# Kernel optimization log

Measured on AMD Instinct MI355X. Metric: run time of the kernel, lower is better.

## Reference

```python
import jax, jax.numpy as jnp
import numpy as np

NEG_SLOPE = 0.2


def add_self_loops(edge_index, num_nodes):
    loop = jnp.arange(num_nodes, dtype=edge_index.dtype)
    src = jnp.concatenate([edge_index[0], loop])
    dst = jnp.concatenate([edge_index[1], loop])
    return src, dst


def gat_conv(x, src, dst, W, att_src, att_dst, bias, heads, out_ch, concat):
    N = x.shape[0]
    h = (x @ W).reshape(N, heads, out_ch)                      # [N,H,C]
    a_src = jnp.sum(h * att_src, axis=-1)                      # [N,H]
    a_dst = jnp.sum(h * att_dst, axis=-1)                      # [N,H]
    e = a_src[src] + a_dst[dst]                                # [E,H]
    e = jax.nn.leaky_relu(e, NEG_SLOPE)
    # segment softmax over incoming edges of each destination node
    m = jax.ops.segment_max(e, dst, num_segments=N)            # [N,H]
    m = jnp.where(jnp.isfinite(m), m, 0.0)
    ex = jnp.exp(e - m[dst])
    s = jax.ops.segment_sum(ex, dst, num_segments=N)           # [N,H]
    alpha = ex / jnp.where(s[dst] > 0, s[dst], 1.0)            # [E,H]
    msg = alpha[:, :, None] * h[src]                           # [E,H,C]
    out = jax.ops.segment_sum(msg, dst, num_segments=N)        # [N,H,C]
    if concat:
        out = out.reshape(N, heads * out_ch)
    else:
        out = out.mean(axis=1)
    return out + bias


def setup_inputs() -> dict:
    key = jax.random.key(0)
    ks = jax.random.split(key, 10)
    N, F, E, H, C1 = 50000, 128, 800000, 8, 8
    x = jax.random.normal(ks[0], (N, F), dtype=jnp.float32)
    edge_index = jax.random.randint(ks[1], (2, E), 0, N, dtype=jnp.int64)
    sc = 0.1
    W1 = jax.random.normal(ks[2], (F, H * C1), dtype=jnp.float32) * sc
    a_src1 = jax.random.normal(ks[3], (H, C1), dtype=jnp.float32) * sc
    a_dst1 = jax.random.normal(ks[4], (H, C1), dtype=jnp.float32) * sc
    b1 = jnp.zeros((H * C1,), dtype=jnp.float32)
    W2 = jax.random.normal(ks[5], (H * C1, F), dtype=jnp.float32) * sc
    a_src2 = jax.random.normal(ks[6], (1, F), dtype=jnp.float32) * sc
    a_dst2 = jax.random.normal(ks[7], (1, F), dtype=jnp.float32) * sc
    b2 = jnp.zeros((F,), dtype=jnp.float32)
    return {"x": x, "edge_index": edge_index, "W1": W1, "a_src1": a_src1,
            "a_dst1": a_dst1, "b1": b1, "W2": W2, "a_src2": a_src2,
            "a_dst2": a_dst2, "b2": b2}


def reference(x, edge_index, W1, a_src1, a_dst1, b1, W2, a_src2, a_dst2, b2):
    N = x.shape[0]
    src, dst = add_self_loops(edge_index, N)
    h = gat_conv(x, src, dst, W1, a_src1, a_dst1, b1, heads=8, out_ch=8, concat=True)
    h = jax.nn.elu(h)
    out = gat_conv(h, src, dst, W2, a_src2, a_dst2, b2, heads=1, out_ch=x.shape[1], concat=True)
    return out
```

## Files before the change

### kernel.cpp

```cpp
#include <hip/hip_runtime.h>
#include <hip/hip_fp16.h>
#include <math.h>

#define NEG_SLOPE 0.2f

typedef _Float16 f16x8 __attribute__((ext_vector_type(8)));
typedef float    f32x4 __attribute__((ext_vector_type(4)));

__device__ __forceinline__ void get_edge(const int* __restrict__ ei, int E, int e,
                                         int& s, int& d) {
    if (e < E) { s = ei[e]; d = ei[E + e]; }
    else       { s = e - E; d = e - E; }
}

union G1SMem {
    unsigned int sWu[4096];
    struct {
        int lhist[256], lbase[256], lrank[256];
        unsigned int sbuf[4096];
    } sc;
};

__global__ __launch_bounds__(256) void g1s_kernel(const float* __restrict__ x,
                                                  const float* __restrict__ W,
                                                  const float* __restrict__ asrc,
                                                  const float* __restrict__ adst,
                                                  _Float16* __restrict__ hout,
                                                  float* __restrict__ av,
                                                  float* __restrict__ bv, int N,
                                                  int gblocks,
                                                  const float* __restrict__ W2,
                                                  const float* __restrict__ as2,
                                                  const float* __restrict__ ad2,
                                                  float* __restrict__ wa,
                                                  float* __restrict__ wb,
                                                  const int* __restrict__ ei, int E, int ET,
                                                  unsigned int* __restrict__ bstore,
                                                  int* __restrict__ bofs) {
    __shared__ G1SMem sm;
    int t = threadIdx.x;

    if (blockIdx.x == (unsigned)gblocks) {
        if (t < 64) {
            const float* wr = W2 + t * 128;
            float sa = 0.f, sb = 0.f;
#pragma unroll 8
            for (int c = 0; c < 128; ++c) {
                float w = wr[c];
                sa = fmaf(w, as2[c], sa);
                sb = fmaf(w, ad2[c], sb);
            }
            wa[t] = sa; wb[t] = sb;
        }
        return;
    }

    if (blockIdx.x > (unsigned)gblocks) {
        int sblk = blockIdx.x - gblocks - 1;
        int start = sblk * 4096;
        int cnt = ET - start; if (cnt > 4096) cnt = 4096;
        sm.sc.lhist[t] = 0; sm.sc.lrank[t] = 0;
        __syncthreads();
        int mybuck[16]; unsigned int myval[16];
#pragma unroll
        for (int k = 0; k < 16; ++k) {
            int e = start + t + k * 256;
            mybuck[k] = -1;
            if (e < ET) {
                int s, d; get_edge(ei, E, e, s, d);
                mybuck[k] = d >> 8;
                myval[k] = ((unsigned int)(d & 255) << 16) | (unsigned int)s;
                atomicAdd(&sm.sc.lhist[mybuck[k]], 1);
            }
        }
        __syncthreads();
        int v = sm.sc.lhist[t];
        sm.sc.lbase[t] = v;
        __syncthreads();
        for (int off = 1; off < 256; off <<= 1) {
            int u = (t >= off) ? sm.sc.lbase[t - off] : 0;
            __syncthreads();
            sm.sc.lbase[t] += u;
            __syncthreads();
        }
        int excl = sm.sc.lbase[t] - v;
        bofs[(sblk << 8) + t] = excl;
        sm.sc.lbase[t] = excl;
        __syncthreads();
#pragma unroll
        for (int k = 0; k < 16; ++k) {
            int b = mybuck[k];
            if (b >= 0) {
                int r = atomicAdd(&sm.sc.lrank[b], 1);
                sm.sc.sbuf[sm.sc.lbase[b] + r] = myval[k];
            }
        }
        __syncthreads();
        for (int j = t; j < cnt; j += 256)
            bstore[start + j] = sm.sc.sbuf[j];
        return;
    }

    for (int p = t; p < 4096; p += 256) {
        int frag = p >> 8;
        int lane = (p >> 2) & 63;
        int j2   = p & 3;
        int chunk = frag >> 2, nt = frag & 3;
        int k = chunk * 32 + ((lane >> 4) << 3) + (j2 << 1);
        int n = nt * 16 + (lane & 15);
        union { _Float16 h[2]; unsigned int u; } pk;
        pk.h[0] = (_Float16)W[k * 64 + n];
        pk.h[1] = (_Float16)W[(k + 1) * 64 + n];
        sm.sWu[p] = pk.u;
    }
    __syncthreads();

    int lane = t & 63;
    int wid  = t >> 6;
    int rbase = blockIdx.x * 64 + wid * 16;
    int l15 = lane & 15, quad = lane >> 4;
    int rA = rbase + l15; if (rA >= N) rA = N - 1;

    const unsigned int* fragbase = &sm.sWu[lane * 4];
    f32x4 z = {0.f, 0.f, 0.f, 0.f};
    f32x4 acc[4] = {z, z, z, z};

#pragma unroll
    for (int chunk = 0; chunk < 4; ++chunk) {
        const float* xp = x + (size_t)rA * 128 + chunk * 32 + quad * 8;
        float4 f0 = *((const float4*)xp);
        float4 f1 = *((const float4*)(xp + 4));
        f16x8 af;
        af[0] = (_Float16)f0.x; af[1] = (_Float16)f0.y;
        af[2] = (_Float16)f0.z; af[3] = (_Float16)f0.w;
        af[4] = (_Float16)f1.x; af[5] = (_Float16)f1.y;
        af[6] = (_Float16)f1.z; af[7] = (_Float16)f1.w;
#pragma unroll
        for (int tt = 0; tt < 4; ++tt) {
            f16x8 bf = *((const f16x8*)(fragbase + (chunk * 4 + tt) * 256));
            acc[tt] = __builtin_amdgcn_mfma_f32_16x16x32_f16(af, bf, acc[tt], 0, 0, 0);
        }
    }

    float asc[4], adc[4];
#pragma unroll
    for (int tt = 0; tt < 4; ++tt) { asc[tt] = asrc[tt * 16 + l15]; adc[tt] = adst[tt * 16 + l15]; }
#pragma unroll
    for (int reg = 0; reg < 4; ++reg) {
        int r = rbase + quad * 4 + reg;
        bool ok = (r < N);
#pragma unroll
        for (int tt = 0; tt < 4; ++tt) {
            float v = acc[tt][reg];
            if (ok) hout[(size_t)r * 64 + tt * 16 + l15] = (_Float16)v;
            float pa = v * asc[tt], pb = v * adc[tt];
            pa += __shfl_xor(pa, 1); pb += __shfl_xor(pb, 1);
            pa += __shfl_xor(pa, 2); pb += __shfl_xor(pb, 2);
            pa += __shfl_xor(pa, 4); pb += __shfl_xor(pb, 4);
            if (ok && (lane & 7) == 0) {
                int head = tt * 2 + (l15 >> 3);
                av[r * 8 + head] = pa;
                bv[r * 8 + head] = pb;
            }
        }
    }
}

__device__ __forceinline__ void rank_quarter(const unsigned int* __restrict__ bstore,
                                             const int* __restrict__ bofs,
                                             int b, int q, int ET, int nblk,
                                             unsigned short (*colL)[64],
                                             int* lrank) {
    int t = threadIdx.x;
    if (t < 64) lrank[t] = 0;
    __syncthreads();
    int lane = t & 63, wid = t >> 6;
    for (int sblk = wid; sblk < nblk; sblk += 8) {
        int base = sblk << 12;
        int cnt = ET - base; if (cnt > 4096) cnt = 4096;
        int beg = bofs[(sblk << 8) + b];
        int end = (b < 255) ? bofs[(sblk << 8) + b + 1] : cnt;
        for (int i = beg + lane; i < end; i += 64) {
            unsigned int pk = bstore[base + i];
            int local = pk >> 16;
            if ((local >> 6) == q) {
                int r = atomicAdd(&lrank[local & 63], 1);
                if (r < 64) colL[local & 63][r] = (unsigned short)(pk & 0xFFFFu);
            }
        }
    }
    __syncthreads();
}

__global__ __launch_bounds__(512) void agg1_kernel(const unsigned int* __restrict__ bstore,
                                                   const int* __restrict__ bofs,
                                                   const float* __restrict__ av,
                                                   const float* __restrict__ bv,
                                                   const __half* __restrict__ h1,
                                                   const float* __restrict__ b1,
                                                   const float* __restrict__ wa,
                                                   const float* __restrict__ wb,
                                                   _Float16* __restrict__ out1,
                                                   float* __restrict__ av2,
                                                   float* __restrict__ bv2,
                                                   int N, int ET, int nblk) {
    __shared__ unsigned short colL[64][64];
    __shared__ int lrank[64];
    int blk = blockIdx.x;
    rank_quarter(bstore, bofs, blk >> 2, blk & 3, ET, nblk, colL, lrank);

    int lane = threadIdx.x & 63;
    int wid  = threadIdx.x >> 6;
    int g  = (lane >> 3) & 3;
    int gl = lane & 7;
    const uint4* hrow = (const uint4*)h1;
    uint4 z4 = {0u, 0u, 0u, 0u};

#pragma unroll 1
    for (int pass = 0; pass < 4; ++pass) {
        int nl = pass * 16 + wid * 2 + (lane >> 5);
        int node = blk * 64 + nl;
        bool valid = node < N;
        int nodeC = valid ? node : 0;
        int deg = lrank[nl]; if (deg > 64) deg = 64;
        int last = deg - 1; if (last < 0) last = 0;
        float bd = bv[nodeC * 8 + gl];

        int e = g;
        int c0 = colL[nl][e      <= last ? e      : last];
        int c1 = colL[nl][e + 4  <= last ? e + 4  : last];
        int c2 = colL[nl][e + 8  <= last ? e + 8  : last];
        float av0 = 0.f, av1v = 0.f; uint4 h0 = z4, h1v = z4;
        if (e < deg)     { av0  = av[c0 * 8 + gl]; h0  = hrow[(size_t)c0 * 8 + gl]; }
        if (e + 4 < deg) { av1v = av[c1 * 8 + gl]; h1v = hrow[(size_t)c1 * 8 + gl]; }

        float s = 0.f, a0 = 0.f, a1 = 0.f, a2 = 0.f, a3 = 0.f,
              a4 = 0.f, a5 = 0.f, a6 = 0.f, a7 = 0.f;
        for (; e < deg; e += 4) {
            float av2v = 0.f; uint4 h2 = z4;
            if (e + 8 < deg) { av2v = av[c2 * 8 + gl]; h2 = hrow[(size_t)c2 * 8 + gl]; }
            int c3 = colL[nl][e + 12 <= last ? e + 12 : last];
            float l = av0 + bd;
            l = l > 0.f ? l : NEG_SLOPE * l;
            float w = __expf(l);
            float2 f0 = __half22float2(*(const __half2*)&h0.x);
            float2 f1 = __half22float2(*(const __half2*)&h0.y);
            float2 f2 = __half22float2(*(const __half2*)&h0.z);
            float2 f3 = __half22float2(*(const __half2*)&h0.w);
            s += w;
            a0 = fmaf(w, f0.x, a0); a1 = fmaf(w, f0.y, a1);
            a2 = fmaf(w, f1.x, a2); a3 = fmaf(w, f1.y, a3);
            a4 = fmaf(w, f2.x, a4); a5 = fmaf(w, f2.y, a5);
            a6 = fmaf(w, f3.x, a6); a7 = fmaf(w, f3.y, a7);
            av0 = av1v; h0 = h1v; av1v = av2v; h1v = h2; c2 = c3;
        }
#pragma unroll
        for (int off = 8; off < 32; off <<= 1) {
            s  += __shfl_xor(s, off);
            a0 += __shfl_xor(a0, off); a1 += __shfl_xor(a1, off);
            a2 += __shfl_xor(a2, off); a3 += __shfl_xor(a3, off);
            a4 += __shfl_xor(a4, off); a5 += __shfl_xor(a5, off);
            a6 += __shfl_xor(a6, off); a7 += __shfl_xor(a7, off);
        }
        float inv = s > 0.f ? __builtin_amdgcn_rcpf(s) : 0.f;
        float4 bb0 = ((const float4*)b1)[gl * 2];
        float4 bb1 = ((const float4*)b1)[gl * 2 + 1];
        float v0 = a0 * inv + bb0.x, v1 = a1 * inv + bb0.y;
        float v2 = a2 * inv + bb0.z, v3 = a3 * inv + bb0.w;
        float v4 = a4 * inv + bb1.x, v5 = a5 * inv + bb1.y;
        float v6 = a6 * inv + bb1.z, v7 = a7 * inv + bb1.w;
        v0 = v0 > 0.f ? v0 : __expf(v0) - 1.f; v1 = v1 > 0.f ? v1 : __expf(v1) - 1.f;
        v2 = v2 > 0.f ? v2 : __expf(v2) - 1.f; v3 = v3 > 0.f ? v3 : __expf(v3) - 1.f;
        v4 = v4 > 0.f ? v4 : __expf(v4) - 1.f; v5 = v5 > 0.f ? v5 : __expf(v5) - 1.f;
        v6 = v6 > 0.f ? v6 : __expf(v6) - 1.f; v7 = v7 > 0.f ? v7 : __expf(v7) - 1.f;
        float4 wa0 = ((const float4*)wa)[gl * 2], wa1 = ((const float4*)wa)[gl * 2 + 1];
        float4 wb0 = ((const float4*)wb)[gl * 2], wb1 = ((const float4*)wb)[gl * 2 + 1];
        float pa = v0 * wa0.x + v1 * wa0.y + v2 * wa0.z + v3 * wa0.w
                 + v4 * wa1.x + v5 * wa1.y + v6 * wa1.z + v7 * wa1.w;
        float pb = v0 * wb0.x + v1 * wb0.y + v2 * wb0.z + v3 * wb0.w
                 + v4 * wb1.x + v5 * wb1.y + v6 * wb1.z + v7 * wb1.w;
        pa += __shfl_xor(pa, 1); pb += __shfl_xor(pb, 1);
        pa += __shfl_xor(pa, 2); pb += __shfl_xor(pb, 2);
        pa += __shfl_xor(pa, 4); pb += __shfl_xor(pb, 4);
        if (valid && (lane & 31) == 0) { av2[node] = pa; bv2[node] = pb; }
        if (valid && g == 0) {
            f16x8 o;
            o[0] = (_Float16)v0; o[1] = (_Float16)v1; o[2] = (_Float16)v2; o[3] = (_Float16)v3;
            o[4] = (_Float16)v4; o[5] = (_Float16)v5; o[6] = (_Float16)v6; o[7] = (_Float16)v7;
            ((f16x8*)out1)[(size_t)node * 8 + gl] = o;
        }
    }
}

union A2Mem {
    struct { unsigned short colL[64][64]; int lrank[64]; } rk;
    unsigned int sWu[4096];
};

__global__ __launch_bounds__(512) void agg2g2_kernel(const unsigned int* __restrict__ bstore,
                                                     const int* __restrict__ bofs,
                                                     const float* __restrict__ av,
                                                     const float* __restrict__ bv,
                                                     const __half* __restrict__ out1,
                                                     const float* __restrict__ W,
                                                     const float* __restrict__ b2,
                                                     float* __restrict__ dout,
                                                     int N, int ET, int nblk) {
    __shared__ A2Mem sm;
    __shared__ _Float16 sAgg[64][72];
    int blk = blockIdx.x;
    int t = threadIdx.x;
    int lane = t & 63;
    int wid  = t >> 6;
    int rbase = blk * 64;

    rank_quarter(bstore, bofs, blk >> 2, blk & 3, ET, nblk, sm.rk.colL, sm.rk.lrank);

    int g  = (lane >> 3) & 3;
    int gl = lane & 7;
    const uint4* hrow = (const uint4*)out1;
    uint4 z4 = {0u, 0u, 0u, 0u};
#pragma unroll 1
    for (int pass = 0; pass < 4; ++pass) {
        int nl = pass * 16 + wid * 2 + (lane >> 5);
        int node = rbase + nl;
        bool valid = node < N;
        int nodeC = valid ? node : 0;
        int deg = sm.rk.lrank[nl]; if (deg > 64) deg = 64;
        int last = deg - 1; if (last < 0) last = 0;
        float bd = bv[nodeC];

        int e = g;
        int c0 = sm.rk.colL[nl][e      <= last ? e      : last];
        int c1 = sm.rk.colL[nl][e + 4  <= last ? e + 4  : last];
        int c2 = sm.rk.colL[nl][e + 8  <= last ? e + 8  : last];
        float av0 = 0.f, av1v = 0.f; uint4 h0 = z4, h1v = z4;
        if (e < deg)     { av0  = av[c0]; h0  = hrow[(size_t)c0 * 8 + gl]; }
        if (e + 4 < deg) { av1v = av[c1]; h1v = hrow[(size_t)c1 * 8 + gl]; }

        float s = 0.f, a0 = 0.f, a1 = 0.f, a2 = 0.f, a3 = 0.f,
              a4 = 0.f, a5 = 0.f, a6 = 0.f, a7 = 0.f;
        for (; e < deg; e += 4) {
            float av2v = 0.f; uint4 h2 = z4;
            if (e + 8 < deg) { av2v = av[c2]; h2 = hrow[(size_t)c2 * 8 + gl]; }
            int c3 = sm.rk.colL[nl][e + 12 <= last ? e + 12 : last];
            float l = av0 + bd;
            l = l > 0.f ? l : NEG_SLOPE * l;
            float w = __expf(l);
            float2 f0 = __half22float2(*(const __half2*)&h0.x);
            float2 f1 = __half22float2(*(const __half2*)&h0.y);
            float2 f2 = __half22float2(*(const __half2*)&h0.z);
            float2 f3 = __half22float2(*(const __half2*)&h0.w);
            s += w;
            a0 = fmaf(w, f0.x, a0); a1 = fmaf(w, f0.y, a1);
            a2 = fmaf(w, f1.x, a2); a3 = fmaf(w, f1.y, a3);
            a4 = fmaf(w, f2.x, a4); a5 = fmaf(w, f2.y, a5);
            a6 = fmaf(w, f3.x, a6); a7 = fmaf(w, f3.y, a7);
            av0 = av1v; h0 = h1v; av1v = av2v; h1v = h2; c2 = c3;
        }
#pragma unroll
        for (int off = 8; off < 32; off <<= 1) {
            s  += __shfl_xor(s, off);
            a0 += __shfl_xor(a0, off); a1 += __shfl_xor(a1, off);
            a2 += __shfl_xor(a2, off); a3 += __shfl_xor(a3, off);
            a4 += __shfl_xor(a4, off); a5 += __shfl_xor(a5, off);
            a6 += __shfl_xor(a6, off); a7 += __shfl_xor(a7, off);
        }
        if (g == 0) {
            float inv = s > 0.f ? __builtin_amdgcn_rcpf(s) : 0.f;
            f16x8 o;
            o[0] = (_Float16)(a0 * inv); o[1] = (_Float16)(a1 * inv);
            o[2] = (_Float16)(a2 * inv); o[3] = (_Float16)(a3 * inv);
            o[4] = (_Float16)(a4 * inv); o[5] = (_Float16)(a5 * inv);
            o[6] = (_Float16)(a6 * inv); o[7] = (_Float16)(a7 * inv);
            *((f16x8*)&sAgg[nl][gl * 8]) = o;
        }
    }
    __syncthreads();

    for (int p = t; p < 4096; p += 512) {
        int frag = p >> 8;
        int ln = (p >> 2) & 63;
        int j2 = p & 3;
        int chunk = frag >> 3, nt = frag & 7;
        int k = chunk * 32 + ((ln >> 4) << 3) + (j2 << 1);
        int n = nt * 16 + (ln & 15);
        union { _Float16 h[2]; unsigned int u; } pk;
        pk.h[0] = (_Float16)W[k * 128 + n];
        pk.h[1] = (_Float16)W[(k + 1) * 128 + n];
        sm.sWu[p] = pk.u;
    }
    __syncthreads();

    int rblk = (wid & 3) * 16;
    int chalf = wid >> 2;
    int l15 = lane & 15, quad = lane >> 4;

    const unsigned int* fragbase = &sm.sWu[lane * 4];
    f32x4 z = {0.f, 0.f, 0.f, 0.f};
    f32x4 acc[4] = {z, z, z, z};

#pragma unroll
    for (int chunk = 0; chunk < 2; ++chunk) {
        f16x8 af = *((const f16x8*)&sAgg[rblk + l15][chunk * 32 + quad * 8]);
#pragma unroll
        for (int tt = 0; tt < 4; ++tt) {
            f16x8 bf = *((const f16x8*)(fragbase + (chunk * 8 + chalf * 4 + tt) * 256));
            acc[tt] = __builtin_amdgcn_mfma_f32_16x16x32_f16(af, bf, acc[tt], 0, 0, 0);
        }
    }

    float bcol[4];
#pragma unroll
    for (int tt = 0; tt < 4; ++tt) bcol[tt] = b2[chalf * 64 + tt * 16 + l15];
#pragma unroll
    for (int reg = 0; reg < 4; ++reg) {
        int r = rbase + rblk + quad * 4 + reg;
        if (r < N) {
#pragma unroll
            for (int tt = 0; tt < 4; ++tt)
                dout[(size_t)r * 128 + chalf * 64 + tt * 16 + l15] = acc[tt][reg] + bcol[tt];
        }
    }
}

extern "C" void kernel_launch(void* const* d_in, const int* in_sizes, int n_in,
                              void* d_out, int out_size, void* d_ws, size_t ws_size,
                              hipStream_t stream) {
    const float* x      = (const float*)d_in[0];
    const int*   ei     = (const int*)  d_in[1];
    const float* W1     = (const float*)d_in[2];
    const float* a_src1 = (const float*)d_in[3];
    const float* a_dst1 = (const float*)d_in[4];
    const float* b1     = (const float*)d_in[5];
    const float* W2     = (const float*)d_in[6];
    const float* a_src2 = (const float*)d_in[7];
    const float* a_dst2 = (const float*)d_in[8];
    const float* b2     = (const float*)d_in[9];
    float* dout = (float*)d_out;

    const int N  = in_sizes[0] / 128;
    const int E  = in_sizes[1] / 2;
    const int ET = E + N;
    const int NBLKA = (ET + 4095) >> 12;
    const int NB64  = (N + 63) >> 6;

    char* wsb = (char*)d_ws;
    _Float16* h1     = (_Float16*)wsb; wsb += (size_t)N * 64 * 2;
    _Float16* out1   = (_Float16*)wsb; wsb += (size_t)N * 64 * 2;
    float* av1  = (float*)wsb; wsb += (size_t)N * 8 * 4;
    float* bv1  = (float*)wsb; wsb += (size_t)N * 8 * 4;
    float* av2  = (float*)wsb; wsb += (size_t)N * 4;
    float* bv2  = (float*)wsb; wsb += (size_t)N * 4;
    float* wa   = (float*)wsb; wsb += 64 * 4;
    float* wb   = (float*)wsb; wsb += 64 * 4;
    unsigned int* bstore = (unsigned int*)wsb; wsb += (size_t)NBLKA * 4096 * 4;
    int* bofs   = (int*)wsb; wsb += (size_t)NBLKA * 256 * 4;

    const int gblocks = (N + 63) / 64;

    g1s_kernel<<<gblocks + 1 + NBLKA, 256, 0, stream>>>(x, W1, a_src1, a_dst1, h1, av1, bv1, N,
                                                        gblocks, W2, a_src2, a_dst2, wa, wb,
                                                        ei, E, ET, bstore, bofs);

    agg1_kernel<<<NB64, 512, 0, stream>>>(bstore, bofs, av1, bv1,
                                          (const __half*)h1, b1, wa, wb,
                                          out1, av2, bv2, N, ET, NBLKA);

    agg2g2_kernel<<<NB64, 512, 0, stream>>>(bstore, bofs, av2, bv2,
                                            (const __half*)out1, W2, b2, dout,
                                            N, ET, NBLKA);
}
```

Baseline: 211.6 us.

## Fuse GAT pipeline into cooperative persistent megakernel with global bucket CSR build

Replaces the three separate kernels with one persistent cooperative kernel that runs phases (GEMM+scatter, CSR build, layer-1 aggregation, layer-2 aggregation+GEMM) separated by grid syncs. The edge bucketing now writes into global per-bucket regions via atomic cursors, and a dedicated CSR phase materialises per-node column lists so aggregation no longer rescans every scatter block's bucket slice. Attention logits are pre-scaled by log2(e) so exp2 can be used. This removes per-block redundant rank scans and launch gaps, but adds grid-sync cost, a memset, fixed bucket capacity and 64-degree truncation limits, and a fallback multi-launch path.

Measured after the change: 376.5 us. 1.78x slower.

```diff
diff --git a/kernel.cpp b/kernel.cpp
--- a/kernel.cpp
+++ b/kernel.cpp
@@ -1,11 +1,42 @@
 #include <hip/hip_runtime.h>
+#include <hip/hip_cooperative_groups.h>
 #include <hip/hip_fp16.h>
 #include <math.h>
 
+namespace cg = cooperative_groups;
+
 #define NEG_SLOPE 0.2f
+#define BSTRIDE 6144
+#define L2E 1.4426950408889634f
 
 typedef _Float16 f16x8 __attribute__((ext_vector_type(8)));
 typedef float    f32x4 __attribute__((ext_vector_type(4)));
+
+struct MP {
+    const float *x, *W1, *asrc, *adst;
+    _Float16 *h1;
+    float *av1, *bv1;
+    int N, tiles128;
+    const float *W2, *as2, *ad2;
+    float *wa, *wb;
+    int *bcur;
+    const int *ei; int E, ET;
+    unsigned int *bstore; int nbuck, nblka;
+    int *cnt; unsigned short *col;
+    const float *b1;
+    _Float16 *out1;
+    float *av2, *bv2;
+    const float *b2;
+    float *dout;
+    int nitems16;
+};
+
+union MegaSMem {
+    unsigned int sWu[4096];
+    struct { int lhist[256], lbase[256], lrank[256], gbase[256];
+             unsigned int sbuf[4096]; int saddr[4096]; } sc;
+    struct { int lrank[256]; } csr;
+};
 
 __device__ __forceinline__ void get_edge(const int* __restrict__ ei, int E, int e,
                                          int& s, int& d) {
@@ -13,113 +44,24 @@
     else       { s = e - E; d = e - E; }
 }
 
-union G1SMem {
-    unsigned int sWu[4096];
-    struct {
-        int lhist[256], lbase[256], lrank[256];
-        unsigned int sbuf[4096];
-    } sc;
-};
-
-__global__ __launch_bounds__(256) void g1s_kernel(const float* __restrict__ x,
-                                                  const float* __restrict__ W,
-                                                  const float* __restrict__ asrc,
-                                                  const float* __restrict__ adst,
-                                                  _Float16* __restrict__ hout,
-                                                  float* __restrict__ av,
-                                                  float* __restrict__ bv, int N,
-                                                  int gblocks,
-                                                  const float* __restrict__ W2,
-                                                  const float* __restrict__ as2,
-                                                  const float* __restrict__ ad2,
-                                                  float* __restrict__ wa,
-                                                  float* __restrict__ wb,
-                                                  const int* __restrict__ ei, int E, int ET,
-                                                  unsigned int* __restrict__ bstore,
-                                                  int* __restrict__ bofs) {
-    __shared__ G1SMem sm;
-    int t = threadIdx.x;
-
-    if (blockIdx.x == (unsigned)gblocks) {
-        if (t < 64) {
-            const float* wr = W2 + t * 128;
-            float sa = 0.f, sb = 0.f;
-#pragma unroll 8
-            for (int c = 0; c < 128; ++c) {
-                float w = wr[c];
-                sa = fmaf(w, as2[c], sa);
-                sb = fmaf(w, ad2[c], sb);
-            }
-            wa[t] = sa; wb[t] = sb;
-        }
-        return;
-    }
-
-    if (blockIdx.x > (unsigned)gblocks) {
-        int sblk = blockIdx.x - gblocks - 1;
-        int start = sblk * 4096;
-        int cnt = ET - start; if (cnt > 4096) cnt = 4096;
-        sm.sc.lhist[t] = 0; sm.sc.lrank[t] = 0;
-        __syncthreads();
-        int mybuck[16]; unsigned int myval[16];
-#pragma unroll
-        for (int k = 0; k < 16; ++k) {
-            int e = start + t + k * 256;
-            mybuck[k] = -1;
-            if (e < ET) {
-                int s, d; get_edge(ei, E, e, s, d);
-                mybuck[k] = d >> 8;
-                myval[k] = ((unsigned int)(d & 255) << 16) | (unsigned int)s;
-                atomicAdd(&sm.sc.lhist[mybuck[k]], 1);
-            }
-        }
-        __syncthreads();
-        int v = sm.sc.lhist[t];
-        sm.sc.lbase[t] = v;
-        __syncthreads();
-        for (int off = 1; off < 256; off <<= 1) {
-            int u = (t >= off) ? sm.sc.lbase[t - off] : 0;
-            __syncthreads();
-            sm.sc.lbase[t] += u;
-            __syncthreads();
-        }
-        int excl = sm.sc.lbase[t] - v;
-        bofs[(sblk << 8) + t] = excl;
-        sm.sc.lbase[t] = excl;
-        __syncthreads();
-#pragma unroll
-        for (int k = 0; k < 16; ++k) {
-            int b = mybuck[k];
-            if (b >= 0) {
-                int r = atomicAdd(&sm.sc.lrank[b], 1);
-                sm.sc.sbuf[sm.sc.lbase[b] + r] = myval[k];
-            }
-        }
-        __syncthreads();
-        for (int j = t; j < cnt; j += 256)
-            bstore[start + j] = sm.sc.sbuf[j];
-        return;
-    }
-
-    for (int p = t; p < 4096; p += 256) {
-        int frag = p >> 8;
-        int lane = (p >> 2) & 63;
-        int j2   = p & 3;
+__device__ void gemm_tile(MegaSMem& sm, const MP& p, int tile) {
+    int t = threadIdx.x;
+    for (int q = t; q < 4096; q += 512) {
+        int frag = q >> 8, lane = (q >> 2) & 63, j2 = q & 3;
         int chunk = frag >> 2, nt = frag & 3;
         int k = chunk * 32 + ((lane >> 4) << 3) + (j2 << 1);
         int n = nt * 16 + (lane & 15);
         union { _Float16 h[2]; unsigned int u; } pk;
-        pk.h[0] = (_Float16)W[k * 64 + n];
-        pk.h[1] = (_Float16)W[(k + 1) * 64 + n];
-        sm.sWu[p] = pk.u;
-    }
-    __syncthreads();
-
-    int lane = t & 63;
-    int wid  = t >> 6;
-    int rbase = blockIdx.x * 64 + wid * 16;
+        pk.h[0] = (_Float16)p.W1[k * 64 + n];
+        pk.h[1] = (_Float16)p.W1[(k + 1) * 64 + n];
+        sm.sWu[q] = pk.u;
+    }
+    __syncthreads();
+
+    int lane = t & 63, wid = t >> 6;
+    int rbase = tile * 128 + wid * 16;
     int l15 = lane & 15, quad = lane >> 4;
-    int rA = rbase + l15; if (rA >= N) rA = N - 1;
+    int rA = rbase + l15; if (rA >= p.N) rA = p.N - 1;
 
     const unsigned int* fragbase = &sm.sWu[lane * 4];
     f32x4 z = {0.f, 0.f, 0.f, 0.f};
@@ -127,7 +69,7 @@
 
 #pragma unroll
     for (int chunk = 0; chunk < 4; ++chunk) {
-        const float* xp = x + (size_t)rA * 128 + chunk * 32 + quad * 8;
+        const float* xp = p.x + (size_t)rA * 128 + chunk * 32 + quad * 8;
         float4 f0 = *((const float4*)xp);
         float4 f1 = *((const float4*)(xp + 4));
         f16x8 af;
@@ -144,105 +86,250 @@
 
     float asc[4], adc[4];
 #pragma unroll
-    for (int tt = 0; tt < 4; ++tt) { asc[tt] = asrc[tt * 16 + l15]; adc[tt] = adst[tt * 16 + l15]; }
+    for (int tt = 0; tt < 4; ++tt) {
+        asc[tt] = p.asrc[tt * 16 + l15] * L2E;
+        adc[tt] = p.adst[tt * 16 + l15] * L2E;
+    }
 #pragma unroll
     for (int reg = 0; reg < 4; ++reg) {
         int r = rbase + quad * 4 + reg;
-        bool ok = (r < N);
+        bool ok = (r < p.N);
 #pragma unroll
         for (int tt = 0; tt < 4; ++tt) {
             float v = acc[tt][reg];
-            if (ok) hout[(size_t)r * 64 + tt * 16 + l15] = (_Float16)v;
+            if (ok) p.h1[(size_t)r * 64 + tt * 16 + l15] = (_Float16)v;
             float pa = v * asc[tt], pb = v * adc[tt];
             pa += __shfl_xor(pa, 1); pb += __shfl_xor(pb, 1);
             pa += __shfl_xor(pa, 2); pb += __shfl_xor(pb, 2);
             pa += __shfl_xor(pa, 4); pb += __shfl_xor(pb, 4);
             if (ok && (lane & 7) == 0) {
                 int head = tt * 2 + (l15 >> 3);
-                av[r * 8 + head] = pa;
-                bv[r * 8 + head] = pb;
+                p.av1[r * 8 + head] = pa;
+                p.bv1[r * 8 + head] = pb;
             }
         }
     }
-}
-
-__device__ __forceinline__ void rank_quarter(const unsigned int* __restrict__ bstore,
-                                             const int* __restrict__ bofs,
-                                             int b, int q, int ET, int nblk,
-                                             unsigned short (*colL)[64],
-                                             int* lrank) {
-    int t = threadIdx.x;
-    if (t < 64) lrank[t] = 0;
-    __syncthreads();
-    int lane = t & 63, wid = t >> 6;
-    for (int sblk = wid; sblk < nblk; sblk += 8) {
-        int base = sblk << 12;
-        int cnt = ET - base; if (cnt > 4096) cnt = 4096;
-        int beg = bofs[(sblk << 8) + b];
-        int end = (b < 255) ? bofs[(sblk << 8) + b + 1] : cnt;
-        for (int i = beg + lane; i < end; i += 64) {
-            unsigned int pk = bstore[base + i];
-            int local = pk >> 16;
-            if ((local >> 6) == q) {
-                int r = atomicAdd(&lrank[local & 63], 1);
-                if (r < 64) colL[local & 63][r] = (unsigned short)(pk & 0xFFFFu);
-            }
-        }
-    }
-    __syncthreads();
-}
-
-__global__ __launch_bounds__(512) void agg1_kernel(const unsigned int* __restrict__ bstore,
-                                                   const int* __restrict__ bofs,
-                                                   const float* __restrict__ av,
-                                                   const float* __restrict__ bv,
-                                                   const __half* __restrict__ h1,
-                                                   const float* __restrict__ b1,
-                                                   const float* __restrict__ wa,
-                                                   const float* __restrict__ wb,
-                                                   _Float16* __restrict__ out1,
-                                                   float* __restrict__ av2,
-                                                   float* __restrict__ bv2,
-                                                   int N, int ET, int nblk) {
-    __shared__ unsigned short colL[64][64];
-    __shared__ int lrank[64];
-    int blk = blockIdx.x;
-    rank_quarter(bstore, bofs, blk >> 2, blk & 3, ET, nblk, colL, lrank);
-
-    int lane = threadIdx.x & 63;
-    int wid  = threadIdx.x >> 6;
+    __syncthreads();
+}
+
+__device__ void aux_unit(const MP& p) {
+    int t = threadIdx.x;
+    if (t < 64) {
+        const float* wr = p.W2 + t * 128;
+        float sa = 0.f, sb = 0.f;
+#pragma unroll 8
+        for (int c = 0; c < 128; ++c) {
+            float w = wr[c];
+            sa = fmaf(w, p.as2[c], sa);
+            sb = fmaf(w, p.ad2[c], sb);
+        }
+        p.wa[t] = sa * L2E; p.wb[t] = sb * L2E;
+    }
+}
+
+__device__ void scatter_chunk(MegaSMem& sm, const MP& p, int sblk) {
+    int t = threadIdx.x;
+    int start = sblk * 4096;
+    int cnt_ = p.ET - start; if (cnt_ > 4096) cnt_ = 4096;
+    if (t < 256) { sm.sc.lhist[t] = 0; sm.sc.lrank[t] = 0; }
+    __syncthreads();
+    int mybuck[8]; unsigned int myval[8];
+#pragma unroll
+    for (int k = 0; k < 8; ++k) {
+        int e = start + t + k * 512;
+        mybuck[k] = -1;
+        if (e < p.ET) {
+            int s, d; get_edge(p.ei, p.E, e, s, d);
+            mybuck[k] = d >> 8;
+            myval[k] = ((unsigned int)d << 16) | (unsigned int)s;
+            atomicAdd(&sm.sc.lhist[mybuck[k]], 1);
+        }
+    }
+    __syncthreads();
+    int v = 0;
+    if (t < 256) { v = sm.sc.lhist[t]; sm.sc.lbase[t] = v; }
+    __syncthreads();
+    for (int off = 1; off < 256; off <<= 1) {
+        int u = (t >= off && t < 256) ? sm.sc.lbase[t - off] : 0;
+        __syncthreads();
+        if (t < 256) sm.sc.lbase[t] += u;
+        __syncthreads();
+    }
+    if (t < 256) {
+        int excl = sm.sc.lbase[t] - v;
+        if (t < p.nbuck && v > 0)
+            sm.sc.gbase[t] = t * BSTRIDE + atomicAdd(&p.bcur[t], v);
+        sm.sc.lbase[t] = excl;
+    }
+    __syncthreads();
+#pragma unroll
+    for (int k = 0; k < 8; ++k) {
+        int b = mybuck[k];
+        if (b >= 0) {
+            int r = atomicAdd(&sm.sc.lrank[b], 1);
+            int idx = sm.sc.lbase[b] + r;
+            sm.sc.sbuf[idx] = myval[k];
+            sm.sc.saddr[idx] = sm.sc.gbase[b] + r;
+        }
+    }
+    __syncthreads();
+    for (int j = t; j < cnt_; j += 512)
+        p.bstore[sm.sc.saddr[j]] = sm.sc.sbuf[j];
+    __syncthreads();
+}
+
+__device__ void csr_item(MegaSMem& sm, const MP& p, int b) {
+    int t = threadIdx.x;
+    int base = b * BSTRIDE;
+    int nb = p.bcur[b]; if (nb > BSTRIDE) nb = BSTRIDE;
+    if (t < 256) sm.csr.lrank[t] = 0;
+    __syncthreads();
+    for (int i = t; i < nb; i += 512) {
+        unsigned int pk = p.bstore[base + i];
+        int local = (pk >> 16) & 255;
+        int r = atomicAdd(&sm.csr.lrank[local], 1);
+        if (r < 64) p.col[(size_t)(((b << 8) + local) << 6) + r] =
+                        (unsigned short)(pk & 0xFFFFu);
+    }
+    __syncthreads();
+    int node = (b << 8) + t;
+    if (t < 256 && node < p.N) {
+        int deg = sm.csr.lrank[t]; if (deg > 64) deg = 64;
+        p.cnt[node] = deg;
+    }
+    __syncthreads();
+}
+
+__device__ void agg1_item(const MP& p, int item) {
+    int t = threadIdx.x;
+    int lane = t & 63;
+    int node = item * 16 + (t >> 6) * 2 + (lane >> 5);
+    bool valid = node < p.N;
+    int nodeC = valid ? node : 0;
     int g  = (lane >> 3) & 3;
     int gl = lane & 7;
-    const uint4* hrow = (const uint4*)h1;
+    const unsigned short* colp = p.col + ((size_t)nodeC << 6);
+    int deg = p.cnt[nodeC];
+    int last = deg - 1; if (last < 0) last = 0;
+    float bd = p.bv1[nodeC * 8 + gl];
+    const uint4* hrow = (const uint4*)p.h1;
+
     uint4 z4 = {0u, 0u, 0u, 0u};
-
-#pragma unroll 1
-    for (int pass = 0; pass < 4; ++pass) {
-        int nl = pass * 16 + wid * 2 + (lane >> 5);
-        int node = blk * 64 + nl;
-        bool valid = node < N;
+    int e = g;
+    int c0 = colp[e      <= last ? e      : last];
+    int c1 = colp[e + 4  <= last ? e + 4  : last];
+    int c2 = colp[e + 8  <= last ? e + 8  : last];
+    float av0 = 0.f, av1v = 0.f; uint4 h0 = z4, h1v = z4;
+    if (e < deg)     { av0  = p.av1[c0 * 8 + gl]; h0  = hrow[(size_t)c0 * 8 + gl]; }
+    if (e + 4 < deg) { av1v = p.av1[c1 * 8 + gl]; h1v = hrow[(size_t)c1 * 8 + gl]; }
+
+    float s = 0.f, a0 = 0.f, a1 = 0.f, a2 = 0.f, a3 = 0.f,
+          a4 = 0.f, a5 = 0.f, a6 = 0.f, a7 = 0.f;
+    for (; e < deg; e += 4) {
+        float av2v = 0.f; uint4 h2 = z4;
+        if (e + 8 < deg) { av2v = p.av1[c2 * 8 + gl]; h2 = hrow[(size_t)c2 * 8 + gl]; }
+        int c3 = colp[e + 12 <= last ? e + 12 : last];
+        float l = av0 + bd;
+        l = l > 0.f ? l : NEG_SLOPE * l;
+        float w = __builtin_amdgcn_exp2f(l);
+        float2 f0 = __half22float2(*(const __half2*)&h0.x);
+        float2 f1 = __half22float2(*(const __half2*)&h0.y);
+        float2 f2 = __half22float2(*(const __half2*)&h0.z);
+        float2 f3 = __half22float2(*(const __half2*)&h0.w);
+        s += w;
+        a0 = fmaf(w, f0.x, a0); a1 = fmaf(w, f0.y, a1);
+        a2 = fmaf(w, f1.x, a2); a3 = fmaf(w, f1.y, a3);
+        a4 = fmaf(w, f2.x, a4); a5 = fmaf(w, f2.y, a5);
+        a6 = fmaf(w, f3.x, a6); a7 = fmaf(w, f3.y, a7);
+        av0 = av1v; h0 = h1v; av1v = av2v; h1v = h2; c2 = c3;
+    }
+#pragma unroll
+    for (int off = 8; off < 32; off <<= 1) {
+        s  += __shfl_xor(s, off);
+        a0 += __shfl_xor(a0, off); a1 += __shfl_xor(a1, off);
+        a2 += __shfl_xor(a2, off); a3 += __shfl_xor(a3, off);
+        a4 += __shfl_xor(a4, off); a5 += __shfl_xor(a5, off);
+        a6 += __shfl_xor(a6, off); a7 += __shfl_xor(a7, off);
+    }
+    float inv = s > 0.f ? __builtin_amdgcn_rcpf(s) : 0.f;
+    float4 bb0 = ((const float4*)p.b1)[gl * 2];
+    float4 bb1 = ((const float4*)p.b1)[gl * 2 + 1];
+    float v0 = a0 * inv + bb0.x, v1 = a1 * inv + bb0.y;
+    float v2 = a2 * inv + bb0.z, v3 = a3 * inv + bb0.w;
+    float v4 = a4 * inv + bb1.x, v5 = a5 * inv + bb1.y;
+    float v6 = a6 * inv + bb1.z, v7 = a7 * inv + bb1.w;
+    v0 = v0 > 0.f ? v0 : __expf(v0) - 1.f; v1 = v1 > 0.f ? v1 : __expf(v1) - 1.f;
+    v2 = v2 > 0.f ? v2 : __expf(v2) - 1.f; v3 = v3 > 0.f ? v3 : __expf(v3) - 1.f;
+    v4 = v4 > 0.f ? v4 : __expf(v4) - 1.f; v5 = v5 > 0.f ? v5 : __expf(v5) - 1.f;
+    v6 = v6 > 0.f ? v6 : __expf(v6) - 1.f; v7 = v7 > 0.f ? v7 : __expf(v7) - 1.f;
+    float4 wa0 = ((const float4*)p.wa)[gl * 2], wa1 = ((const float4*)p.wa)[gl * 2 + 1];
+    float4 wb0 = ((const float4*)p.wb)[gl * 2], wb1 = ((const float4*)p.wb)[gl * 2 + 1];
+    float pa = v0 * wa0.x + v1 * wa0.y + v2 * wa0.z + v3 * wa0.w
+             + v4 * wa1.x + v5 * wa1.y + v6 * wa1.z + v7 * wa1.w;
+    float pb = v0 * wb0.x + v1 * wb0.y + v2 * wb0.z + v3 * wb0.w
+             + v4 * wb1.x + v5 * wb1.y + v6 * wb1.z + v7 * wb1.w;
+    pa += __shfl_xor(pa, 1); pb += __shfl_xor(pb, 1);
+    pa += __shfl_xor(pa, 2); pb += __shfl_xor(pb, 2);
+    pa += __shfl_xor(pa, 4); pb += __shfl_xor(pb, 4);
+    if (valid && (lane & 31) == 0) { p.av2[node] = pa; p.bv2[node] = pb; }
+    if (valid && g == 0) {
+        f16x8 o;
+        o[0] = (_Float16)v0; o[1] = (_Float16)v1; o[2] = (_Float16)v2; o[3] = (_Float16)v3;
+        o[4] = (_Float16)v4; o[5] = (_Float16)v5; o[6] = (_Float16)v6; o[7] = (_Float16)v7;
+        ((f16x8*)p.out1)[(size_t)node * 8 + gl] = o;
+    }
+}
+
+__device__ void phaseD(MegaSMem& sm, _Float16 (*sAgg)[72], const MP& p) {
+    int t = threadIdx.x;
+    for (int q = t; q < 4096; q += 512) {
+        int frag = q >> 8, ln = (q >> 2) & 63, j2 = q & 3;
+        int chunk = frag >> 3, nt = frag & 7;
+        int k = chunk * 32 + ((ln >> 4) << 3) + (j2 << 1);
+        int n = nt * 16 + (ln & 15);
+        union { _Float16 h[2]; unsigned int u; } pk;
+        pk.h[0] = (_Float16)p.W2[k * 128 + n];
+        pk.h[1] = (_Float16)p.W2[(k + 1) * 128 + n];
+        sm.sWu[q] = pk.u;
+    }
+    __syncthreads();
+
+    int lane = t & 63, wid = t >> 6;
+    int g  = (lane >> 3) & 3;
+    int gl = lane & 7;
+    int l15 = lane & 15, quad = lane >> 4;
+    const uint4* hrow = (const uint4*)p.out1;
+    const unsigned int* fragbase = &sm.sWu[lane * 4];
+    float bcol = p.b2[wid * 16 + l15];
+    uint4 z4 = {0u, 0u, 0u, 0u};
+
+    for (int item = blockIdx.x; item < p.nitems16; item += gridDim.x) {
+        int nl = wid * 2 + (lane >> 5);
+        int node = item * 16 + nl;
+        bool valid = node < p.N;
         int nodeC = valid ? node : 0;
-        int deg = lrank[nl]; if (deg > 64) deg = 64;
+        const unsigned short* colp = p.col + ((size_t)nodeC << 6);
+        int deg = p.cnt[nodeC];
         int last = deg - 1; if (last < 0) last = 0;
-        float bd = bv[nodeC * 8 + gl];
+        float bd = p.bv2[nodeC];
 
         int e = g;
-        int c0 = colL[nl][e      <= last ? e      : last];
-        int c1 = colL[nl][e + 4  <= last ? e + 4  : last];
-        int c2 = colL[nl][e + 8  <= last ? e + 8  : last];
+        int c0 = colp[e      <= last ? e      : last];
+        int c1 = colp[e + 4  <= last ? e + 4  : last];
+        int c2 = colp[e + 8  <= last ? e + 8  : last];
         float av0 = 0.f, av1v = 0.f; uint4 h0 = z4, h1v = z4;
-        if (e < deg)     { av0  = av[c0 * 8 + gl]; h0  = hrow[(size_t)c0 * 8 + gl]; }
-        if (e + 4 < deg) { av1v = av[c1 * 8 + gl]; h1v = hrow[(size_t)c1 * 8 + gl]; }
+        if (e < deg)     { av0  = p.av2[c0]; h0  = hrow[(size_t)c0 * 8 + gl]; }
+        if (e + 4 < deg) { av1v = p.av2[c1]; h1v = hrow[(size_t)c1 * 8 + gl]; }
 
         float s = 0.f, a0 = 0.f, a1 = 0.f, a2 = 0.f, a3 = 0.f,
               a4 = 0.f, a5 = 0.f, a6 = 0.f, a7 = 0.f;
         for (; e < deg; e += 4) {
             float av2v = 0.f; uint4 h2 = z4;
-            if (e + 8 < deg) { av2v = av[c2 * 8 + gl]; h2 = hrow[(size_t)c2 * 8 + gl]; }
-            int c3 = colL[nl][e + 12 <= last ? e + 12 : last];
+            if (e + 8 < deg) { av2v = p.av2[c2]; h2 = hrow[(size_t)c2 * 8 + gl]; }
+            int c3 = colp[e + 12 <= last ? e + 12 : last];
             float l = av0 + bd;
             l = l > 0.f ? l : NEG_SLOPE * l;
-            float w = __expf(l);
+            float w = __builtin_amdgcn_exp2f(l);
             float2 f0 = __half22float2(*(const __half2*)&h0.x);
             float2 f1 = __half22float2(*(const __half2*)&h0.y);
             float2 f2 = __half22float2(*(const __half2*)&h0.z);
@@ -262,112 +349,8 @@
             a4 += __shfl_xor(a4, off); a5 += __shfl_xor(a5, off);
             a6 += __shfl_xor(a6, off); a7 += __shfl_xor(a7, off);
         }
-        float inv = s > 0.f ? __builtin_amdgcn_rcpf(s) : 0.f;
-        float4 bb0 = ((const float4*)b1)[gl * 2];
-        float4 bb1 = ((const float4*)b1)[gl * 2 + 1];
-        float v0 = a0 * inv + bb0.x, v1 = a1 * inv + bb0.y;
-        float v2 = a2 * inv + bb0.z, v3 = a3 * inv + bb0.w;
-        float v4 = a4 * inv + bb1.x, v5 = a5 * inv + bb1.y;
-        float v6 = a6 * inv + bb1.z, v7 = a7 * inv + bb1.w;
-        v0 = v0 > 0.f ? v0 : __expf(v0) - 1.f; v1 = v1 > 0.f ? v1 : __expf(v1) - 1.f;
-        v2 = v2 > 0.f ? v2 : __expf(v2) - 1.f; v3 = v3 > 0.f ? v3 : __expf(v3) - 1.f;
-        v4 = v4 > 0.f ? v4 : __expf(v4) - 1.f; v5 = v5 > 0.f ? v5 : __expf(v5) - 1.f;
-        v6 = v6 > 0.f ? v6 : __expf(v6) - 1.f; v7 = v7 > 0.f ? v7 : __expf(v7) - 1.f;
-        float4 wa0 = ((const float4*)wa)[gl * 2], wa1 = ((const float4*)wa)[gl * 2 + 1];
-        float4 wb0 = ((const float4*)wb)[gl * 2], wb1 = ((const float4*)wb)[gl * 2 + 1];
-        float pa = v0 * wa0.x + v1 * wa0.y + v2 * wa0.z + v3 * wa0.w
-                 + v4 * wa1.x + v5 * wa1.y + v6 * wa1.z + v7 * wa1.w;
-        float pb = v0 * wb0.x + v1 * wb0.y + v2 * wb0.z + v3 * wb0.w
-                 + v4 * wb1.x + v5 * wb1.y + v6 * wb1.z + v7 * wb1.w;
-        pa += __shfl_xor(pa, 1); pb += __shfl_xor(pb, 1);
-        pa += __shfl_xor(pa, 2); pb += __shfl_xor(pb, 2);
-        pa += __shfl_xor(pa, 4); pb += __shfl_xor(pb, 4);
-        if (valid && (lane & 31) == 0) { av2[node] = pa; bv2[node] = pb; }
-        if (valid && g == 0) {
-            f16x8 o;
-            o[0] = (_Float16)v0; o[1] = (_Float16)v1; o[2] = (_Float16)v2; o[3] = (_Float16)v3;
-            o[4] = (_Float16)v4; o[5] = (_Float16)v5; o[6] = (_Float16)v6; o[7] = (_Float16)v7;
-            ((f16x8*)out1)[(size_t)node * 8 + gl] = o;
-        }
-    }
-}
-
-union A2Mem {
-    struct { unsigned short colL[64][64]; int lrank[64]; } rk;
-    unsigned int sWu[4096];
-};
-
-__global__ __launch_bounds__(512) void agg2g2_kernel(const unsigned int* __restrict__ bstore,
-                                                     const int* __restrict__ bofs,
-                                                     const float* __restrict__ av,
-                                                     const float* __restrict__ bv,
-                                                     const __half* __restrict__ out1,
-                                                     const float* __restrict__ W,
-                                                     const float* __restrict__ b2,
-                                                     float* __restrict__ dout,
-                                                     int N, int ET, int nblk) {
-    __shared__ A2Mem sm;
-    __shared__ _Float16 sAgg[64][72];
-    int blk = blockIdx.x;
-    int t = threadIdx.x;
-    int lane = t & 63;
-    int wid  = t >> 6;
-    int rbase = blk * 64;
-
-    rank_quarter(bstore, bofs, blk >> 2, blk & 3, ET, nblk, sm.rk.colL, sm.rk.lrank);
-
-    int g  = (lane >> 3) & 3;
-    int gl = lane & 7;
-    const uint4* hrow = (const uint4*)out1;
-    uint4 z4 = {0u, 0u, 0u, 0u};
-#pragma unroll 1
-    for (int pass = 0; pass < 4; ++pass) {
-        int nl = pass * 16 + wid * 2 + (lane >> 5);
-        int node = rbase + nl;
-        bool valid = node < N;
-        int nodeC = valid ? node : 0;
-        int deg = sm.rk.lrank[nl]; if (deg > 64) deg = 64;
-        int last = deg - 1; if (last < 0) last = 0;
-        float bd = bv[nodeC];
-
-        int e = g;
-        int c0 = sm.rk.colL[nl][e      <= last ? e      : last];
-        int c1 = sm.rk.colL[nl][e + 4  <= last ? e + 4  : last];
-        int c2 = sm.rk.colL[nl][e + 8  <= last ? e + 8  : last];
-        float av0 = 0.f, av1v = 0.f; uint4 h0 = z4, h1v = z4;
-        if (e < deg)     { av0  = av[c0]; h0  = hrow[(size_t)c0 * 8 + gl]; }
-        if (e + 4 < deg) { av1v = av[c1]; h1v = hrow[(size_t)c1 * 8 + gl]; }
-
-        float s = 0.f, a0 = 0.f, a1 = 0.f, a2 = 0.f, a3 = 0.f,
-              a4 = 0.f, a5 = 0.f, a6 = 0.f, a7 = 0.f;
-        for (; e < deg; e += 4) {
-            float av2v = 0.f; uint4 h2 = z4;
-            if (e + 8 < deg) { av2v = av[c2]; h2 = hrow[(size_t)c2 * 8 + gl]; }
-            int c3 = sm.rk.colL[nl][e + 12 <= last ? e + 12 : last];
-            float l = av0 + bd;
-            l = l > 0.f ? l : NEG_SLOPE * l;
-            float w = __expf(l);
-            float2 f0 = __half22float2(*(const __half2*)&h0.x);
-            float2 f1 = __half22float2(*(const __half2*)&h0.y);
-            float2 f2 = __half22float2(*(const __half2*)&h0.z);
-            float2 f3 = __half22float2(*(const __half2*)&h0.w);
-            s += w;
-            a0 = fmaf(w, f0.x, a0); a1 = fmaf(w, f0.y, a1);
-            a2 = fmaf(w, f1.x, a2); a3 = fmaf(w, f1.y, a3);
-            a4 = fmaf(w, f2.x, a4); a5 = fmaf(w, f2.y, a5);
-            a6 = fmaf(w, f3.x, a6); a7 = fmaf(w, f3.y, a7);
-            av0 = av1v; h0 = h1v; av1v = av2v; h1v = h2; c2 = c3;
-        }
-#pragma unroll
-        for (int off = 8; off < 32; off <<= 1) {
-            s  += __shfl_xor(s, off);
-            a0 += __shfl_xor(a0, off); a1 += __shfl_xor(a1, off);
-            a2 += __shfl_xor(a2, off); a3 += __shfl_xor(a3, off);
-            a4 += __shfl_xor(a4, off); a5 += __shfl_xor(a5, off);
-            a6 += __shfl_xor(a6, off); a7 += __shfl_xor(a7, off);
-        }
         if (g == 0) {
-            float inv = s > 0.f ? __builtin_amdgcn_rcpf(s) : 0.f;
+            float inv = (valid && s > 0.f) ? __builtin_amdgcn_rcpf(s) : 0.f;
             f16x8 o;
             o[0] = (_Float16)(a0 * inv); o[1] = (_Float16)(a1 * inv);
             o[2] = (_Float16)(a2 * inv); o[3] = (_Float16)(a3 * inv);
@@ -375,99 +358,103 @@
             o[6] = (_Float16)(a6 * inv); o[7] = (_Float16)(a7 * inv);
             *((f16x8*)&sAgg[nl][gl * 8]) = o;
         }
-    }
-    __syncthreads();
-
-    for (int p = t; p < 4096; p += 512) {
-        int frag = p >> 8;
-        int ln = (p >> 2) & 63;
-        int j2 = p & 3;
-        int chunk = frag >> 3, nt = frag & 7;
-        int k = chunk * 32 + ((ln >> 4) << 3) + (j2 << 1);
-        int n = nt * 16 + (ln & 15);
-        union { _Float16 h[2]; unsigned int u; } pk;
-        pk.h[0] = (_Float16)W[k * 128 + n];
-        pk.h[1] = (_Float16)W[(k + 1) * 128 + n];
-        sm.sWu[p] = pk.u;
-    }
-    __syncthreads();
-
-    int rblk = (wid & 3) * 16;
-    int chalf = wid >> 2;
-    int l15 = lane & 15, quad = lane >> 4;
-
-    const unsigned int* fragbase = &sm.sWu[lane * 4];
-    f32x4 z = {0.f, 0.f, 0.f, 0.f};
-    f32x4 acc[4] = {z, z, z, z};
-
-#pragma unroll
-    for (int chunk = 0; chunk < 2; ++chunk) {
-        f16x8 af = *((const f16x8*)&sAgg[rblk + l15][chunk * 32 + quad * 8]);
-#pragma unroll
-        for (int tt = 0; tt < 4; ++tt) {
-            f16x8 bf = *((const f16x8*)(fragbase + (chunk * 8 + chalf * 4 + tt) * 256));
-            acc[tt] = __builtin_amdgcn_mfma_f32_16x16x32_f16(af, bf, acc[tt], 0, 0, 0);
-        }
-    }
-
-    float bcol[4];
-#pragma unroll
-    for (int tt = 0; tt < 4; ++tt) bcol[tt] = b2[chalf * 64 + tt * 16 + l15];
-#pragma unroll
-    for (int reg = 0; reg < 4; ++reg) {
-        int r = rbase + rblk + quad * 4 + reg;
-        if (r < N) {
-#pragma unroll
-            for (int tt = 0; tt < 4; ++tt)
-                dout[(size_t)r * 128 + chalf * 64 + tt * 16 + l15] = acc[tt][reg] + bcol[tt];
-        }
+        __syncthreads();
+
+        f32x4 acc = {0.f, 0.f, 0.f, 0.f};
+#pragma unroll
+        for (int chunk = 0; chunk < 2; ++chunk) {
+            f16x8 af = *((const f16x8*)&sAgg[l15][chunk * 32 + quad * 8]);
+            f16x8 bf = *((const f16x8*)(fragbase + (chunk * 8 + wid) * 256));
+            acc = __builtin_amdgcn_mfma_f32_16x16x32_f16(af, bf, acc, 0, 0, 0);
+        }
+#pragma unroll
+        for (int reg = 0; reg < 4; ++reg) {
+            int r = item * 16 + quad * 4 + reg;
+            if (r < p.N)
+                p.dout[(size_t)r * 128 + wid * 16 + l15] = acc[reg] + bcol;
+        }
+        __syncthreads();
+    }
+}
+
+__global__ __launch_bounds__(512, 4) void mega_kernel(MP p, int phase) {
+    __shared__ MegaSMem sm;
+    __shared__ _Float16 sAgg[16][72];
+
+    if (phase < 0 || phase == 0) {
+        int UA = p.tiles128 + 1 + p.nblka;
+        for (int u = blockIdx.x; u < UA; u += gridDim.x) {
+            if (u < p.tiles128)       gemm_tile(sm, p, u);
+            else if (u == p.tiles128) aux_unit(p);
+            else                      scatter_chunk(sm, p, u - p.tiles128 - 1);
+        }
+    }
+    if (phase < 0) cg::this_grid().sync();
+    if (phase < 0 || phase == 1) {
+        for (int b = blockIdx.x; b < p.nbuck; b += gridDim.x)
+            csr_item(sm, p, b);
+    }
+    if (phase < 0) cg::this_grid().sync();
+    if (phase < 0 || phase == 2) {
+        for (int item = blockIdx.x; item < p.nitems16; item += gridDim.x)
+            agg1_item(p, item);
+    }
+    if (phase < 0) cg::this_grid().sync();
+    if (phase < 0 || phase == 3) {
+        phaseD(sm, sAgg, p);
     }
 }
 
 extern "C" void kernel_launch(void* const* d_in, const int* in_sizes, int n_in,
                               void* d_out, int out_size, void* d_ws, size_t ws_size,
                               hipStream_t stream) {
-    const float* x      = (const float*)d_in[0];
-    const int*   ei     = (const int*)  d_in[1];
-    const float* W1     = (const float*)d_in[2];
-    const float* a_src1 = (const float*)d_in[3];
-    const float* a_dst1 = (const float*)d_in[4];
-    const float* b1     = (const float*)d_in[5];
-    const float* W2     = (const float*)d_in[6];
-    const float* a_src2 = (const float*)d_in[7];
-    const float* a_dst2 = (const float*)d_in[8];
-    const float* b2     = (const float*)d_in[9];
-    float* dout = (float*)d_out;
-
-    const int N  = in_sizes[0] / 128;
-    const int E  = in_sizes[1] / 2;
-    const int ET = E + N;
-    const int NBLKA = (ET + 4095) >> 12;
-    const int NB64  = (N + 63) >> 6;
+    MP p;
+    p.x      = (const float*)d_in[0];
+    p.ei     = (const int*)  d_in[1];
+    p.W1     = (const float*)d_in[2];
+    p.asrc   = (const float*)d_in[3];
+    p.adst   = (const float*)d_in[4];
+    p.b1     = (const float*)d_in[5];
+    p.W2     = (const float*)d_in[6];
+    p.as2    = (const float*)d_in[7];
+    p.ad2    = (const float*)d_in[8];
+    p.b2     = (const float*)d_in[9];
+    p.dout   = (float*)d_out;
+
+    p.N  = in_sizes[0] / 128;
+    p.E  = in_sizes[1] / 2;
+    p.ET = p.E + p.N;
+    p.nbuck   = (p.N + 255) >> 8;
+    p.nblka   = (p.ET + 4095) >> 12;
+    p.tiles128 = (p.N + 127) >> 7;
+    p.nitems16 = (p.N + 15) >> 4;
 
     char* wsb = (char*)d_ws;
-    _Float16* h1     = (_Float16*)wsb; wsb += (size_t)N * 64 * 2;
-    _Float16* out1   = (_Float16*)wsb; wsb += (size_t)N * 64 * 2;
-    float* av1  = (float*)wsb; wsb += (size_t)N * 8 * 4;
-    float* bv1  = (float*)wsb; wsb += (size_t)N * 8 * 4;
-    float* av2  = (float*)wsb; wsb += (size_t)N * 4;
-    float* bv2  = (float*)wsb; wsb += (size_t)N * 4;
-    float* wa   = (float*)wsb; wsb += 64 * 4;
-    float* wb   = (float*)wsb; wsb += 64 * 4;
-    unsigned int* bstore = (unsigned int*)wsb; wsb += (size_t)NBLKA * 4096 * 4;
-    int* bofs   = (int*)wsb; wsb += (size_t)NBLKA * 256 * 4;
-
-    const int gblocks = (N + 63) / 64;
-
-    g1s_kernel<<<gblocks + 1 + NBLKA, 256, 0, stream>>>(x, W1, a_src1, a_dst1, h1, av1, bv1, N,
-                                                        gblocks, W2, a_src2, a_dst2, wa, wb,
-                                                        ei, E, ET, bstore, bofs);
-
-    agg1_kernel<<<NB64, 512, 0, stream>>>(bstore, bofs, av1, bv1,
-                                          (const __half*)h1, b1, wa, wb,
-                                          out1, av2, bv2, N, ET, NBLKA);
-
-    agg2g2_kernel<<<NB64, 512, 0, stream>>>(bstore, bofs, av2, bv2,
-                                            (const __half*)out1, W2, b2, dout,
-                                            N, ET, NBLKA);
-}
+    p.h1   = (_Float16*)wsb; wsb += (size_t)p.N * 64 * 2;
+    p.out1 = (_Float16*)wsb; wsb += (size_t)p.N * 64 * 2;
+    p.av1  = (float*)wsb; wsb += (size_t)p.N * 8 * 4;
+    p.bv1  = (float*)wsb; wsb += (size_t)p.N * 8 * 4;
+    p.av2  = (float*)wsb; wsb += (size_t)p.N * 4;
+    p.bv2  = (float*)wsb; wsb += (size_t)p.N * 4;
+    p.wa   = (float*)wsb; wsb += 64 * 4;
+    p.wb   = (float*)wsb; wsb += 64 * 4;
+    p.cnt  = (int*)wsb; wsb += (size_t)p.N * 4;
+    p.col  = (unsigned short*)wsb; wsb += (size_t)p.N * 64 * 2;
+    p.bstore = (unsigned int*)wsb; wsb += (size_t)p.nbuck * BSTRIDE * 4;
+    p.bcur   = (int*)wsb; wsb += 256 * 4;
+
+    hipMemsetAsync(p.bcur, 0, 256 * sizeof(int), stream);
+
+    int phase = -1;
+    void* args[] = { &p, &phase };
+    hipError_t err = hipLaunchCooperativeKernel((const void*)mega_kernel,
+                                                dim3(512), dim3(512),
+                                                args, 0, stream);
+    if (err != hipSuccess) {
+        (void)hipGetLastError();
+        mega_kernel<<<512, 512, 0, stream>>>(p, 0);
+        mega_kernel<<<512, 512, 0, stream>>>(p, 1);
+        mega_kernel<<<512, 512, 0, stream>>>(p, 2);
+        mega_kernel<<<512, 512, 0, stream>>>(p, 3);
+    }
+}
```
